# Performance work log

Measured on AMD Instinct MI355X. Metric: run time of the kernel, lower is better.

The kernel has to match this reference:

```python
import jax, jax.numpy as jnp
import numpy as np

B, LL, LP, D, H, TOPK = 4, 256, 256, 256, 128, 100


def setup_inputs() -> dict:
    key = jax.random.key(0)
    ks = jax.random.split(key, 16)
    s = 0.02
    return {
        "l_tok": jax.random.normal(ks[0], (B, LL, D), jnp.float32),
        "p_tok": jax.random.normal(ks[1], (B, LP, D), jnp.float32),
        "l_pad": jax.random.bernoulli(ks[2], 0.1, (B, LL)),
        "p_pad": jax.random.bernoulli(ks[3], 0.1, (B, LP)),
        "Wl": jax.random.normal(ks[4], (D, D), jnp.float32) * s,
        "bl": jnp.zeros((D,), jnp.float32),
        "Wp": jax.random.normal(ks[5], (D, D), jnp.float32) * s,
        "bp": jnp.zeros((D,), jnp.float32),
        "W1": jax.random.normal(ks[6], (H, 4 * D), jnp.float32) * s,
        "b1": jnp.zeros((H,), jnp.float32),
        "W2": jax.random.normal(ks[7], (H, H), jnp.float32) * s,
        "b2": jnp.zeros((H,), jnp.float32),
        "W3": jax.random.normal(ks[8], (1, H), jnp.float32) * s,
        "b3": jnp.zeros((1,), jnp.float32),
    }


def reference(l_tok, p_tok, l_pad, p_pad, Wl, bl, Wp, bp, W1, b1, W2, b2, W3, b3):
    # Linear projections (torch Linear: x @ W.T + b)
    l = jnp.einsum("bld,ed->ble", l_tok, Wl) + bl  # [B,Ll,D]
    p = jnp.einsum("bpd,ed->bpe", p_tok, Wp) + bp  # [B,Lp,D]

    le = jnp.broadcast_to(l[:, :, None, :], (B, LL, LP, D))
    pe = jnp.broadcast_to(p[:, None, :, :], (B, LL, LP, D))
    pair_feat = jnp.concatenate([le, pe, le * pe, jnp.abs(le - pe)], axis=-1)  # [B,Ll,Lp,4D]

    gelu = lambda x: jax.nn.gelu(x, approximate=False)  # torch nn.GELU default (erf)
    h = gelu(jnp.einsum("blpf,hf->blph", pair_feat, W1) + b1)
    h = gelu(jnp.einsum("blph,gh->blpg", h, W2) + b2)
    pair_logit = (jnp.einsum("blph,oh->blpo", h, W3) + b3)[..., 0]  # [B,Ll,Lp]

    pair_logit = jnp.nan_to_num(pair_logit, nan=0.0, posinf=20.0, neginf=-20.0)

    valid = (~l_pad)[:, :, None] & (~p_pad)[:, None, :]  # [B,Ll,Lp]
    pair_logit = jnp.where(valid, pair_logit, -20.0)
    pair_prob = jax.nn.sigmoid(pair_logit)

    flat = pair_logit.reshape(B, -1)
    k_top = min(TOPK, LL * LP)
    topv, _ = jax.lax.top_k(flat, k_top)  # [B,k]
    w = jax.nn.softmax(topv, axis=-1)
    logit = jnp.sum(w * topv, axis=-1)  # [B]
    return logit, pair_logit, pair_prob
```

## Files before the change

### kernel.cpp

```cpp
#include <hip/hip_runtime.h>

#define BB 4
#define LLL 256
#define LPP 256
#define DDIM 256
#define HH 128

typedef _Float16 f16;
typedef f16 f16x8 __attribute__((ext_vector_type(8)));
typedef f16 f16x4 __attribute__((ext_vector_type(4)));
typedef float floatx4 __attribute__((ext_vector_type(4)));

__device__ __forceinline__ float gelu_f(float x) {
    return x * __builtin_amdgcn_rcpf(1.f + __expf(-1.702f * x));
}
__device__ __forceinline__ float sigmoid_f(float x) {
    return __builtin_amdgcn_rcpf(1.f + __expf(-x));
}
__device__ __forceinline__ f16x8 habs8(f16x8 v) {
    uint4 u = __builtin_bit_cast(uint4, v);
    u.x &= 0x7fff7fffu; u.y &= 0x7fff7fffu; u.z &= 0x7fff7fffu; u.w &= 0x7fff7fffu;
    return __builtin_bit_cast(f16x8, u);
}
__device__ __forceinline__ unsigned okey(float f) {
    unsigned u = __float_as_uint(f);
    return (u & 0x80000000u) ? ~u : (u | 0x80000000u);
}

__global__ __launch_bounds__(256) void prep_proj(
    const float* __restrict__ l_tok, const float* __restrict__ p_tok,
    const float* __restrict__ Wl, const float* __restrict__ Wp,
    const float* __restrict__ bl, const float* __restrict__ bp,
    f16* __restrict__ proj) {
    __shared__ __align__(16) char sm[2 * 64 * 80];
    f16* As = (f16*)sm;
    f16* Bs = (f16*)(sm + 64 * 80);
    int tid = threadIdx.x;
    int m0 = blockIdx.x * 64, n0 = blockIdx.y * 64;
    bool isP = (m0 >= 1024);
    const float* Asrc = isP ? (p_tok + (size_t)(m0 - 1024) * DDIM) : (l_tok + (size_t)m0 * DDIM);
    const float* Wsrc = isP ? Wp : Wl;
    const float* bias = isP ? bp : bl;
    int row = tid >> 2, seg = tid & 3;
    int w = tid >> 6, lane = tid & 63;
    int m16 = lane & 15, quad = lane >> 4;
    int wm = w & 1, wn = w >> 1;
    floatx4 acc[2][2];
#pragma unroll
    for (int a = 0; a < 2; ++a)
#pragma unroll
        for (int c = 0; c < 2; ++c) acc[a][c] = (floatx4)0.f;
    for (int k0 = 0; k0 < DDIM; k0 += 32) {
        float4 f0 = *(const float4*)(Asrc + row * DDIM + k0 + seg * 8);
        float4 f1 = *(const float4*)(Asrc + row * DDIM + k0 + seg * 8 + 4);
        f16x8 av;
        av[0] = (f16)f0.x; av[1] = (f16)f0.y; av[2] = (f16)f0.z; av[3] = (f16)f0.w;
        av[4] = (f16)f1.x; av[5] = (f16)f1.y; av[6] = (f16)f1.z; av[7] = (f16)f1.w;
        *(f16x8*)(As + row * 40 + seg * 8) = av;
        float4 g0 = *(const float4*)(Wsrc + (n0 + row) * DDIM + k0 + seg * 8);
        float4 g1 = *(const float4*)(Wsrc + (n0 + row) * DDIM + k0 + seg * 8 + 4);
        f16x8 bv;
        bv[0] = (f16)g0.x; bv[1] = (f16)g0.y; bv[2] = (f16)g0.z; bv[3] = (f16)g0.w;
        bv[4] = (f16)g1.x; bv[5] = (f16)g1.y; bv[6] = (f16)g1.z; bv[7] = (f16)g1.w;
        *(f16x8*)(Bs + row * 40 + seg * 8) = bv;
        __syncthreads();
        f16x8 afr[2], bfr[2];
#pragma unroll
        for (int t = 0; t < 2; ++t)
            afr[t] = *(const f16x8*)(As + (wm * 32 + t * 16 + m16) * 40 + quad * 8);
#pragma unroll
        for (int t = 0; t < 2; ++t)
            bfr[t] = *(const f16x8*)(Bs + (wn * 32 + t * 16 + m16) * 40 + quad * 8);
#pragma unroll
        for (int a = 0; a < 2; ++a)
#pragma unroll
            for (int c = 0; c < 2; ++c)
                acc[a][c] = __builtin_amdgcn_mfma_f32_16x16x32_f16(afr[a], bfr[c], acc[a][c], 0, 0, 0);
        __syncthreads();
    }
#pragma unroll
    for (int c = 0; c < 2; ++c) {
        int col = n0 + wn * 32 + c * 16 + m16;
        float bv = bias[col];
#pragma unroll
        for (int a = 0; a < 2; ++a) {
            int rbase = m0 + wm * 32 + a * 16 + quad * 4;
#pragma unroll
            for (int i = 0; i < 4; ++i)
                proj[(size_t)(rbase + i) * DDIM + col] = (f16)(acc[a][c][i] + bv);
        }
    }
}

__global__ __launch_bounds__(256) void prep_ab(
    const f16* __restrict__ proj, const float* __restrict__ W1,
    const float* __restrict__ W2, float* __restrict__ ABt,
    f16* __restrict__ w1g, f16* __restrict__ w2g) {
    int tid = threadIdx.x;
    if (blockIdx.x >= 32) {
        int idx = ((blockIdx.x - 32) * 2 + blockIdx.y) * 256 + tid;
        if (idx < 8192) {
            int m16 = idx & 15, quad = (idx >> 4) & 3, th = (idx >> 6) & 7;
            int cd = (idx >> 9) & 1, ds = idx >> 10;
            int h = th * 16 + m16;
            const float* src = W1 + (size_t)h * 1024 + 512 + cd * 256 + ds * 32 + quad * 8;
            f16x8 v;
#pragma unroll
            for (int j = 0; j < 8; ++j) v[j] = (f16)src[j];
            *(f16x8*)(w1g + (size_t)idx * 8) = v;
        } else if (idx < 8192 + 2048) {
            int c = idx - 8192;
            int m16 = c & 15, quad = (c >> 4) & 3, tg = (c >> 6) & 7, ks = c >> 9;
            int g = tg * 16 + m16;
            f16x8 v;
#pragma unroll
            for (int j = 0; j < 8; ++j) v[j] = (f16)W2[g * HH + j * 16 + ks * 4 + quad];
            *(f16x8*)(w2g + (size_t)c * 8) = v;
        }
        return;
    }
    __shared__ __align__(16) char sm[2 * 64 * 80];
    f16* As = (f16*)sm;
    f16* Bs = (f16*)(sm + 64 * 80);
    int m0 = blockIdx.x * 64, n0 = blockIdx.y * 64;
    bool isP = (m0 >= 1024);
    int koff = isP ? 256 : 0;
    int row = tid >> 2, seg = tid & 3;
    int w = tid >> 6, lane = tid & 63;
    int m16 = lane & 15, quad = lane >> 4;
    int wm = w & 1, wn = w >> 1;
    floatx4 acc[2][2];
#pragma unroll
    for (int a = 0; a < 2; ++a)
#pragma unroll
        for (int c = 0; c < 2; ++c) acc[a][c] = (floatx4)0.f;
    for (int k0 = 0; k0 < DDIM; k0 += 32) {
        f16x8 av = *(const f16x8*)(proj + (size_t)(m0 + row) * DDIM + k0 + seg * 8);
        *(f16x8*)(As + row * 40 + seg * 8) = av;
        float4 g0 = *(const float4*)(W1 + (size_t)(n0 + row) * 1024 + koff + k0 + seg * 8);
        float4 g1 = *(const float4*)(W1 + (size_t)(n0 + row) * 1024 + koff + k0 + seg * 8 + 4);
        f16x8 bv;
        bv[0] = (f16)g0.x; bv[1] = (f16)g0.y; bv[2] = (f16)g0.z; bv[3] = (f16)g0.w;
        bv[4] = (f16)g1.x; bv[5] = (f16)g1.y; bv[6] = (f16)g1.z; bv[7] = (f16)g1.w;
        *(f16x8*)(Bs + row * 40 + seg * 8) = bv;
        __syncthreads();
        f16x8 afr[2], bfr[2];
#pragma unroll
        for (int t = 0; t < 2; ++t)
            afr[t] = *(const f16x8*)(As + (wm * 32 + t * 16 + m16) * 40 + quad * 8);
#pragma unroll
        for (int t = 0; t < 2; ++t)
            bfr[t] = *(const f16x8*)(Bs + (wn * 32 + t * 16 + m16) * 40 + quad * 8);
#pragma unroll
        for (int a = 0; a < 2; ++a)
#pragma unroll
            for (int c = 0; c < 2; ++c)
                acc[a][c] = __builtin_amdgcn_mfma_f32_16x16x32_f16(afr[a], bfr[c], acc[a][c], 0, 0, 0);
        __syncthreads();
    }
#pragma unroll
    for (int c = 0; c < 2; ++c) {
        int col = n0 + wn * 32 + c * 16 + m16;
#pragma unroll
        for (int a = 0; a < 2; ++a) {
            int rbase = m0 + wm * 32 + a * 16 + quad * 4;
#pragma unroll
            for (int i = 0; i < 4; ++i)
                ABt[(size_t)col * 2048 + rbase + i] = acc[a][c][i];
        }
    }
}

#define H1_STRIDE 272
#define SM_PLOG 139264
#define SM_TOTAL 141312

__global__ __launch_bounds__(512, 2) void pair_main(
    const f16* __restrict__ proj, const float* __restrict__ ABt,
    const f16* __restrict__ w1g, const f16* __restrict__ w2g,
    const float* __restrict__ b1, const float* __restrict__ b2,
    const float* __restrict__ W3, const float* __restrict__ b3,
    const int* __restrict__ l_pad, const int* __restrict__ p_pad,
    float* __restrict__ out) {
    __shared__ __align__(16) char sm[SM_TOTAL];
    int tid = threadIdx.x;
    int lane = tid & 63, w = tid >> 6;
    int m16 = lane & 15, quad = lane >> 4;
    int wp = w & 3, wh = w >> 2;
    int p0 = wp * 64, h0 = wh * 64;
    int b = blockIdx.y;
    int l0 = blockIdx.x * 2;
    int ml0 = b * LLL + l0;
    float* outPL = out + 4;
    float* outPR = out + 4 + BB * LLL * LPP;

    bool pad0 = (l_pad[ml0] != 0), pad1 = (l_pad[ml0 + 1] != 0);
    if (pad0 && pad1) {
        float pr = sigmoid_f(-20.f);
        if (tid < 512) {
            int j = tid >> 8, p = tid & 255;
            outPL[(size_t)(ml0 + j) * LPP + p] = -20.f;
            outPR[(size_t)(ml0 + j) * LPP + p] = pr;
        }
        return;
    }

    float* plog = (float*)(sm + SM_PLOG);

#pragma unroll
    for (int r = 0; r < 16; ++r) {
        int c = tid + r * 512;
        *(f16x8*)(sm + c * 16) = *(const f16x8*)(w1g + (size_t)c * 8);
    }
    if (tid < 512) plog[tid] = 0.f;

    floatx4 acc[2][4][4];
    {
        float av[2][4];
#pragma unroll
        for (int th = 0; th < 4; ++th) {
            int hh = h0 + th * 16 + m16;
            float base = b1[hh];
            av[0][th] = ABt[(size_t)hh * 2048 + ml0] + base;
            av[1][th] = ABt[(size_t)hh * 2048 + ml0 + 1] + base;
        }
#pragma unroll
        for (int tp = 0; tp < 4; ++tp) {
            int rp = p0 + tp * 16 + quad * 4;
#pragma unroll
            for (int th = 0; th < 4; ++th) {
                int hh = h0 + th * 16 + m16;
                floatx4 bp4 = *(const floatx4*)(ABt + (size_t)hh * 2048 + 1024 + b * LPP + rp);
#pragma unroll
                for (int j = 0; j < 2; ++j) {
                    floatx4 a;
#pragma unroll
                    for (int i = 0; i < 4; ++i) a[i] = bp4[i] + av[j][th];
                    acc[j][tp][th] = a;
                }
            }
        }
    }
    __syncthreads();

    {
        const f16* Lr0 = proj + (size_t)ml0 * DDIM + quad * 8;
        const f16* Lr1 = Lr0 + DDIM;
        const f16* Prl[4];
#pragma unroll
        for (int tp = 0; tp < 4; ++tp)
            Prl[tp] = proj + (size_t)(1024 + b * LPP + p0 + tp * 16 + m16) * DDIM + quad * 8;

        f16x8 lv0 = *(const f16x8*)(Lr0);
        f16x8 lv1 = *(const f16x8*)(Lr1);
        f16x8 pv[4];
#pragma unroll
        for (int tp = 0; tp < 4; ++tp) pv[tp] = *(const f16x8*)(Prl[tp]);

        for (int ds = 0; ds < 8; ++ds) {
            f16x8 nlv0, nlv1, npv[4];
            if (ds < 7) {
                nlv0 = *(const f16x8*)(Lr0 + (ds + 1) * 32);
                nlv1 = *(const f16x8*)(Lr1 + (ds + 1) * 32);
#pragma unroll
                for (int tp = 0; tp < 4; ++tp)
                    npv[tp] = *(const f16x8*)(Prl[tp] + (ds + 1) * 32);
            }
            const char* wb = sm + (size_t)(ds * 2) * 8192 + (wh * 4) * 1024 + quad * 256 + m16 * 16;
            {
                f16x8 x[2][4];
#pragma unroll
                for (int tp = 0; tp < 4; ++tp) {
                    x[0][tp] = lv0 * pv[tp];
                    x[1][tp] = lv1 * pv[tp];
                }
#pragma unroll
                for (int th = 0; th < 4; ++th) {
                    f16x8 bf = *(const f16x8*)(wb + th * 1024);
#pragma unroll
                    for (int j = 0; j < 2; ++j)
#pragma unroll
                        for (int tp = 0; tp < 4; ++tp)
                            acc[j][tp][th] = __builtin_amdgcn_mfma_f32_16x16x32_f16(x[j][tp], bf, acc[j][tp][th], 0, 0, 0);
                }
            }
            {
                f16x8 x[2][4];
#pragma unroll
                for (int tp = 0; tp < 4; ++tp) {
                    x[0][tp] = habs8(lv0 - pv[tp]);
                    x[1][tp] = habs8(lv1 - pv[tp]);
                }
#pragma unroll
                for (int th = 0; th < 4; ++th) {
                    f16x8 bf = *(const f16x8*)(wb + 8192 + th * 1024);
#pragma unroll
                    for (int j = 0; j < 2; ++j)
#pragma unroll
                        for (int tp = 0; tp < 4; ++tp)
                            acc[j][tp][th] = __builtin_amdgcn_mfma_f32_16x16x32_f16(x[j][tp], bf, acc[j][tp][th], 0, 0, 0);
                }
            }
            lv0 = nlv0; lv1 = nlv1;
#pragma unroll
            for (int tp = 0; tp < 4; ++tp) pv[tp] = npv[tp];
        }
    }
    __syncthreads();

#pragma unroll
    for (int j = 0; j < 2; ++j) {
        char* h1s = sm + j * (256 * H1_STRIDE);
#pragma unroll
        for (int tp = 0; tp < 4; ++tp) {
#pragma unroll
            for (int i = 0; i < 4; ++i) {
                f16x4 hv;
#pragma unroll
                for (int th = 0; th < 4; ++th) hv[th] = (f16)gelu_f(acc[j][tp][th][i]);
                int p = p0 + tp * 16 + quad * 4 + i;
                *(f16x4*)(h1s + p * H1_STRIDE + m16 * 16 + wh * 8) = hv;
            }
        }
    }
    __syncthreads();

    float b2v[4], w3v[4];
#pragma unroll
    for (int th = 0; th < 4; ++th) {
        int g = h0 + th * 16 + m16;
        b2v[th] = b2[g];
        w3v[th] = W3[g];
    }
    floatx4 acc2[2][4][4];
#pragma unroll
    for (int j = 0; j < 2; ++j)
#pragma unroll
        for (int tp = 0; tp < 4; ++tp)
#pragma unroll
            for (int th = 0; th < 4; ++th) {
                floatx4 a;
                a[0] = a[1] = a[2] = a[3] = b2v[th];
                acc2[j][tp][th] = a;
            }
#pragma unroll
    for (int ks = 0; ks < 4; ++ks) {
        f16x8 af[2][4];
#pragma unroll
        for (int j = 0; j < 2; ++j)
#pragma unroll
            for (int tp = 0; tp < 4; ++tp)
                af[j][tp] = *(const f16x8*)(sm + j * (256 * H1_STRIDE) +
                                            (p0 + tp * 16 + m16) * H1_STRIDE + ks * 64 + quad * 16);
#pragma unroll
        for (int th = 0; th < 4; ++th) {
            f16x8 bf = *(const f16x8*)(w2g + (size_t)(((ks * 8 + wh * 4 + th) * 4 + quad) * 16 + m16) * 8);
#pragma unroll
            for (int j = 0; j < 2; ++j)
#pragma unroll
                for (int tp = 0; tp < 4; ++tp)
                    acc2[j][tp][th] = __builtin_amdgcn_mfma_f32_16x16x32_f16(af[j][tp], bf, acc2[j][tp][th], 0, 0, 0);
        }
    }

#pragma unroll
    for (int j = 0; j < 2; ++j) {
        float part[16];
#pragma unroll
        for (int q = 0; q < 16; ++q) part[q] = 0.f;
#pragma unroll
        for (int tp = 0; tp < 4; ++tp)
#pragma unroll
            for (int th = 0; th < 4; ++th)
#pragma unroll
                for (int i = 0; i < 4; ++i)
                    part[tp * 4 + i] += w3v[th] * gelu_f(acc2[j][tp][th][i]);
#pragma unroll
        for (int mask = 1; mask <= 8; mask <<= 1)
#pragma unroll
            for (int q = 0; q < 16; ++q) part[q] += __shfl_xor(part[q], mask, 64);
        if (m16 == 0) {
#pragma unroll
            for (int tp = 0; tp < 4; ++tp)
#pragma unroll
                for (int i = 0; i < 4; ++i)
                    atomicAdd(&plog[j * 256 + p0 + tp * 16 + quad * 4 + i], part[tp * 4 + i]);
        }
    }
    __syncthreads();

    if (tid < 512) {
        int j = tid >> 8, p = tid & 255;
        int ml = ml0 + j;
        float pl;
        if (l_pad[ml] != 0) {
            pl = -20.f;
        } else {
            pl = plog[tid] + b3[0];
            if (__builtin_isnan(pl)) pl = 0.f;
            else if (__builtin_isinf(pl)) pl = pl > 0.f ? 20.f : -20.f;
            if (p_pad[b * LPP + p] != 0) pl = -20.f;
        }
        outPL[(size_t)ml * LPP + p] = pl;
        outPR[(size_t)ml * LPP + p] = sigmoid_f(pl);
    }
}

#define TK_H0(b) (tk + (b) * 256)
#define TK_H1(b) (tk + 1024 + (b) * 256)
#define TK_SEL(b) (tk + 2048 + (b) * 4)
#define TK_S1(b) ((float*)(tk + 2064) + (b))
#define TK_S2(b) ((float*)(tk + 2068 + 12) + (b))
#define TK_INTS 2096

__global__ __launch_bounds__(256) void tk_hist0(const float* __restrict__ pl,
                                                int* __restrict__ tk) {
    __shared__ int h[256];
    int tid = threadIdx.x, b = blockIdx.y;
    h[tid] = 0;
    __syncthreads();
    float4 t = ((const float4*)(pl + (size_t)b * 65536 + blockIdx.x * 1024))[tid];
#pragma unroll
    for (int c = 0; c < 4; ++c) atomicAdd(&h[okey((&t.x)[c]) >> 24], 1);
    __syncthreads();
    if (h[tid]) atomicAdd(&TK_H0(b)[tid], h[tid]);
}

__global__ __launch_bounds__(256) void tk_sel(int* __restrict__ tk, int level) {
    __shared__ int s[257];
    int tid = threadIdx.x, b = blockIdx.x;
    const int* hsrc = level ? TK_H1(b) : TK_H0(b);
    int K = level ? TK_SEL(b)[1] : 100;
    s[tid] = hsrc[tid];
    __syncthreads();
    for (int off = 1; off < 256; off <<= 1) {
        int v = (tid + off < 256) ? s[tid + off] : 0;
        __syncthreads();
        s[tid] += v;
        __syncthreads();
    }
    int nxt = (tid < 255) ? s[tid + 1] : 0;
    if (s[tid] >= K && nxt < K) {
        TK_SEL(b)[level * 2] = tid;
        TK_SEL(b)[level * 2 + 1] = K - nxt;
    }
}

__global__ __launch_bounds__(256) void tk_pass1(const float* __restrict__ pl,
                                                int* __restrict__ tk) {
    __shared__ int h[256];
    __shared__ float red[8];
    int tid = threadIdx.x, b = blockIdx.y;
    int lane = tid & 63, wv = tid >> 6;
    unsigned pref0 = (unsigned)TK_SEL(b)[0];
    h[tid] = 0;
    __syncthreads();
    float4 t = ((const float4*)(pl + (size_t)b * 65536 + blockIdx.x * 1024))[tid];
    float s1 = 0.f, s2 = 0.f;
#pragma unroll
    for (int c = 0; c < 4; ++c) {
        float v = (&t.x)[c];
        unsigned key = okey(v);
        unsigned hi = key >> 24;
        if (hi > pref0) {
            float e = __expf(v);
            s1 += e;
            s2 += e * v;
        } else if (hi == pref0) {
            atomicAdd(&h[(key >> 16) & 255], 1);
        }
    }
    __syncthreads();
    if (h[tid]) atomicAdd(&TK_H1(b)[tid], h[tid]);
    for (int off = 32; off > 0; off >>= 1) {
        s1 += __shfl_xor(s1, off, 64);
        s2 += __shfl_xor(s2, off, 64);
    }
    if (lane == 0) { red[wv] = s1; red[4 + wv] = s2; }
    __syncthreads();
    if (tid == 0) {
        float a = red[0] + red[1] + red[2] + red[3];
        float bsum = red[4] + red[5] + red[6] + red[7];
        if (a != 0.f) {
            atomicAdd(TK_S1(b), a);
            atomicAdd(TK_S2(b), bsum);
        }
    }
}

__global__ __launch_bounds__(256) void tk_pass2(const float* __restrict__ pl,
                                                int* __restrict__ tk) {
    __shared__ float red[8];
    int tid = threadIdx.x, b = blockIdx.y;
    int lane = tid & 63, wv = tid >> 6;
    unsigned pref0 = (unsigned)TK_SEL(b)[0];
    unsigned pref1 = (unsigned)TK_SEL(b)[2];
    float4 t = ((const float4*)(pl + (size_t)b * 65536 + blockIdx.x * 1024))[tid];
    float s1 = 0.f, s2 = 0.f;
#pragma unroll
    for (int c = 0; c < 4; ++c) {
        float v = (&t.x)[c];
        unsigned key = okey(v);
        if ((key >> 24) == pref0 && ((key >> 16) & 255) > pref1) {
            float e = __expf(v);
            s1 += e;
            s2 += e * v;
        }
    }
    for (int off = 32; off > 0; off >>= 1) {
        s1 += __shfl_xor(s1, off, 64);
        s2 += __shfl_xor(s2, off, 64);
    }
    if (lane == 0) { red[wv] = s1; red[4 + wv] = s2; }
    __syncthreads();
    if (tid == 0) {
        float a = red[0] + red[1] + red[2] + red[3];
        float bsum = red[4] + red[5] + red[6] + red[7];
        if (a != 0.f) {
            atomicAdd(TK_S1(b), a);
            atomicAdd(TK_S2(b), bsum);
        }
    }
}

__global__ __launch_bounds__(64) void tk_fin(int* __restrict__ tk,
                                             float* __restrict__ out) {
    int b = threadIdx.x;
    if (b >= BB) return;
    unsigned pref0 = (unsigned)TK_SEL(b)[0];
    unsigned pref1 = (unsigned)TK_SEL(b)[2];
    int rem1 = TK_SEL(b)[3];
    unsigned key = (pref0 << 24) | (pref1 << 16) | 0x8000u;
    unsigned bits = (key & 0x80000000u) ? (key & 0x7fffffffu) : ~key;
    float vT = __uint_as_float(bits);
    float e = __expf(vT);
    float s1 = *TK_S1(b) + (float)rem1 * e;
    float s2 = *TK_S2(b) + (float)rem1 * e * vT;
    out[b] = s2 * __builtin_amdgcn_rcpf(s1);
}

extern "C" void kernel_launch(void* const* d_in, const int* in_sizes, int n_in,
                              void* d_out, int out_size, void* d_ws, size_t ws_size,
                              hipStream_t stream) {
    const float* l_tok = (const float*)d_in[0];
    const float* p_tok = (const float*)d_in[1];
    const int* l_pad = (const int*)d_in[2];
    const int* p_pad = (const int*)d_in[3];
    const float* Wl = (const float*)d_in[4];
    const float* bl = (const float*)d_in[5];
    const float* Wp = (const float*)d_in[6];
    const float* bp = (const float*)d_in[7];
    const float* W1 = (const float*)d_in[8];
    const float* b1 = (const float*)d_in[9];
    const float* W2 = (const float*)d_in[10];
    const float* b2 = (const float*)d_in[11];
    const float* W3 = (const float*)d_in[12];
    const float* b3 = (const float*)d_in[13];
    float* out = (float*)d_out;

    char* ws = (char*)d_ws;
    f16* proj = (f16*)ws;
    float* ABt = (float*)(ws + (size_t)2048 * 256 * 2);
    f16* w1g = (f16*)(ws + (size_t)2048 * 256 * 2 + (size_t)128 * 2048 * 4);
    f16* w2g = (f16*)((char*)w1g + (size_t)8192 * 16);
    int* tk = (int*)((char*)w2g + (size_t)2048 * 16);

    hipMemsetAsync(tk, 0, TK_INTS * sizeof(int), stream);
    prep_proj<<<dim3(32, 4), 256, 0, stream>>>(l_tok, p_tok, Wl, Wp, bl, bp, proj);
    prep_ab<<<dim3(52, 2), 256, 0, stream>>>(proj, W1, W2, ABt, w1g, w2g);
    pair_main<<<dim3(LLL / 2, BB), 512, 0, stream>>>(proj, ABt, w1g, w2g, b1, b2, W3, b3,
                                                     l_pad, p_pad, out);
    const float* pl = out + 4;
    tk_hist0<<<dim3(64, BB), 256, 0, stream>>>(pl, tk);
    tk_sel<<<BB, 256, 0, stream>>>(tk, 0);
    tk_pass1<<<dim3(64, BB), 256, 0, stream>>>(pl, tk);
    tk_sel<<<BB, 256, 0, stream>>>(tk, 1);
    tk_pass2<<<dim3(64, BB), 256, 0, stream>>>(pl, tk);
    tk_fin<<<1, 64, 0, stream>>>(tk, out);
}
```

Baseline: 178.1 us.

## Fuse top-k histogram into pair kernel and collapse select/finalize launches

The first-level radix histogram moves into pair_main, which builds a per-block shared-memory histogram and flushes it with global atomics. The prefix-scan select step is recomputed redundantly inside each tk_pass block, so the separate tk_hist0, tk_sel and tk_fin kernels are dropped. The final softmax-weighted sum is done by the last block of tk_pass2 using a completion counter, and the workspace memset is folded into extra prep_ab blocks. This removes several small launches and one full re-read of pair_logit, at the cost of extra shared-memory atomics and LDS in the main kernel plus repeated scans in every top-k block.

```diff
diff --git a/kernel.cpp b/kernel.cpp
--- a/kernel.cpp
+++ b/kernel.cpp
@@ -26,6 +26,13 @@
     unsigned u = __float_as_uint(f);
     return (u & 0x80000000u) ? ~u : (u | 0x80000000u);
 }
+
+#define TK_H0(b) (tk + (b) * 256)
+#define TK_H1(b) (tk + 1024 + (b) * 256)
+#define TK_S1(b) ((float*)(tk + 2048) + (b))
+#define TK_S2(b) ((float*)(tk + 2052) + (b))
+#define TK_CNT(b) (tk + 2056 + (b))
+#define TK_INTS 2060
 
 __global__ __launch_bounds__(256) void prep_proj(
     const float* __restrict__ l_tok, const float* __restrict__ p_tok,
@@ -95,7 +102,7 @@
 __global__ __launch_bounds__(256) void prep_ab(
     const f16* __restrict__ proj, const float* __restrict__ W1,
     const float* __restrict__ W2, float* __restrict__ ABt,
-    f16* __restrict__ w1g, f16* __restrict__ w2g) {
+    f16* __restrict__ w1g, f16* __restrict__ w2g, int* __restrict__ tk) {
     int tid = threadIdx.x;
     if (blockIdx.x >= 32) {
         int idx = ((blockIdx.x - 32) * 2 + blockIdx.y) * 256 + tid;
@@ -116,6 +123,9 @@
 #pragma unroll
             for (int j = 0; j < 8; ++j) v[j] = (f16)W2[g * HH + j * 16 + ks * 4 + quad];
             *(f16x8*)(w2g + (size_t)c * 8) = v;
+        } else {
+            int zid = idx - 10240;
+            if (zid >= 0 && zid < TK_INTS) tk[zid] = 0;
         }
         return;
     }
@@ -173,7 +183,8 @@
 
 #define H1_STRIDE 272
 #define SM_PLOG 139264
-#define SM_TOTAL 141312
+#define SM_HIST 141312
+#define SM_TOTAL 142336
 
 __global__ __launch_bounds__(512, 2) void pair_main(
     const f16* __restrict__ proj, const float* __restrict__ ABt,
@@ -181,7 +192,7 @@
     const float* __restrict__ b1, const float* __restrict__ b2,
     const float* __restrict__ W3, const float* __restrict__ b3,
     const int* __restrict__ l_pad, const int* __restrict__ p_pad,
-    float* __restrict__ out) {
+    float* __restrict__ out, int* __restrict__ tk) {
     __shared__ __align__(16) char sm[SM_TOTAL];
     int tid = threadIdx.x;
     int lane = tid & 63, w = tid >> 6;
@@ -202,10 +213,12 @@
             outPL[(size_t)(ml0 + j) * LPP + p] = -20.f;
             outPR[(size_t)(ml0 + j) * LPP + p] = pr;
         }
+        if (tid == 0) atomicAdd(&TK_H0(b)[okey(-20.f) >> 24], 512);
         return;
     }
 
     float* plog = (float*)(sm + SM_PLOG);
+    int* lhist = (int*)(sm + SM_HIST);
 
 #pragma unroll
     for (int r = 0; r < 16; ++r) {
@@ -213,6 +226,7 @@
         *(f16x8*)(sm + c * 16) = *(const f16x8*)(w1g + (size_t)c * 8);
     }
     if (tid < 512) plog[tid] = 0.f;
+    if (tid < 256) lhist[tid] = 0;
 
     floatx4 acc[2][4][4];
     {
@@ -403,58 +417,33 @@
         }
         outPL[(size_t)ml * LPP + p] = pl;
         outPR[(size_t)ml * LPP + p] = sigmoid_f(pl);
-    }
-}
-
-#define TK_H0(b) (tk + (b) * 256)
-#define TK_H1(b) (tk + 1024 + (b) * 256)
-#define TK_SEL(b) (tk + 2048 + (b) * 4)
-#define TK_S1(b) ((float*)(tk + 2064) + (b))
-#define TK_S2(b) ((float*)(tk + 2068 + 12) + (b))
-#define TK_INTS 2096
-
-__global__ __launch_bounds__(256) void tk_hist0(const float* __restrict__ pl,
-                                                int* __restrict__ tk) {
-    __shared__ int h[256];
-    int tid = threadIdx.x, b = blockIdx.y;
-    h[tid] = 0;
-    __syncthreads();
-    float4 t = ((const float4*)(pl + (size_t)b * 65536 + blockIdx.x * 1024))[tid];
-#pragma unroll
-    for (int c = 0; c < 4; ++c) atomicAdd(&h[okey((&t.x)[c]) >> 24], 1);
-    __syncthreads();
-    if (h[tid]) atomicAdd(&TK_H0(b)[tid], h[tid]);
-}
-
-__global__ __launch_bounds__(256) void tk_sel(int* __restrict__ tk, int level) {
-    __shared__ int s[257];
-    int tid = threadIdx.x, b = blockIdx.x;
-    const int* hsrc = level ? TK_H1(b) : TK_H0(b);
-    int K = level ? TK_SEL(b)[1] : 100;
-    s[tid] = hsrc[tid];
-    __syncthreads();
-    for (int off = 1; off < 256; off <<= 1) {
-        int v = (tid + off < 256) ? s[tid + off] : 0;
-        __syncthreads();
-        s[tid] += v;
-        __syncthreads();
-    }
-    int nxt = (tid < 255) ? s[tid + 1] : 0;
-    if (s[tid] >= K && nxt < K) {
-        TK_SEL(b)[level * 2] = tid;
-        TK_SEL(b)[level * 2 + 1] = K - nxt;
-    }
+        atomicAdd(&lhist[okey(pl) >> 24], 1);
+    }
+    __syncthreads();
+    if (tid < 256 && lhist[tid]) atomicAdd(&TK_H0(b)[tid], lhist[tid]);
 }
 
 __global__ __launch_bounds__(256) void tk_pass1(const float* __restrict__ pl,
                                                 int* __restrict__ tk) {
+    __shared__ int s[257];
     __shared__ int h[256];
     __shared__ float red[8];
     int tid = threadIdx.x, b = blockIdx.y;
     int lane = tid & 63, wv = tid >> 6;
-    unsigned pref0 = (unsigned)TK_SEL(b)[0];
+    s[tid] = TK_H0(b)[tid];
     h[tid] = 0;
     __syncthreads();
+    for (int off = 1; off < 256; off <<= 1) {
+        int v = (tid + off < 256) ? s[tid + off] : 0;
+        __syncthreads();
+        s[tid] += v;
+        __syncthreads();
+    }
+    int nxt = (tid < 255) ? s[tid + 1] : 0;
+    if (s[tid] >= 100 && nxt < 100) s[256] = tid;
+    __syncthreads();
+    unsigned pref0 = (unsigned)s[256];
+
     float4 t = ((const float4*)(pl + (size_t)b * 65536 + blockIdx.x * 1024))[tid];
     float s1 = 0.f, s2 = 0.f;
 #pragma unroll
@@ -489,12 +478,44 @@
 }
 
 __global__ __launch_bounds__(256) void tk_pass2(const float* __restrict__ pl,
-                                                int* __restrict__ tk) {
+                                                int* __restrict__ tk,
+                                                float* __restrict__ out) {
+    __shared__ int s[258];
     __shared__ float red[8];
     int tid = threadIdx.x, b = blockIdx.y;
     int lane = tid & 63, wv = tid >> 6;
-    unsigned pref0 = (unsigned)TK_SEL(b)[0];
-    unsigned pref1 = (unsigned)TK_SEL(b)[2];
+    s[tid] = TK_H0(b)[tid];
+    __syncthreads();
+    for (int off = 1; off < 256; off <<= 1) {
+        int v = (tid + off < 256) ? s[tid + off] : 0;
+        __syncthreads();
+        s[tid] += v;
+        __syncthreads();
+    }
+    {
+        int nxt = (tid < 255) ? s[tid + 1] : 0;
+        if (s[tid] >= 100 && nxt < 100) { s[256] = tid; s[257] = 100 - nxt; }
+    }
+    __syncthreads();
+    unsigned pref0 = (unsigned)s[256];
+    int rem0 = s[257];
+    __syncthreads();
+    s[tid] = TK_H1(b)[tid];
+    __syncthreads();
+    for (int off = 1; off < 256; off <<= 1) {
+        int v = (tid + off < 256) ? s[tid + off] : 0;
+        __syncthreads();
+        s[tid] += v;
+        __syncthreads();
+    }
+    {
+        int nxt = (tid < 255) ? s[tid + 1] : 0;
+        if (s[tid] >= rem0 && nxt < rem0) { s[256] = tid; s[257] = rem0 - nxt; }
+    }
+    __syncthreads();
+    unsigned pref1 = (unsigned)s[256];
+    int rem1 = s[257];
+
     float4 t = ((const float4*)(pl + (size_t)b * 65536 + blockIdx.x * 1024))[tid];
     float s1 = 0.f, s2 = 0.f;
 #pragma unroll
@@ -520,23 +541,20 @@
             atomicAdd(TK_S1(b), a);
             atomicAdd(TK_S2(b), bsum);
         }
-    }
-}
-
-__global__ __launch_bounds__(64) void tk_fin(int* __restrict__ tk,
-                                             float* __restrict__ out) {
-    int b = threadIdx.x;
-    if (b >= BB) return;
-    unsigned pref0 = (unsigned)TK_SEL(b)[0];
-    unsigned pref1 = (unsigned)TK_SEL(b)[2];
-    int rem1 = TK_SEL(b)[3];
-    unsigned key = (pref0 << 24) | (pref1 << 16) | 0x8000u;
-    unsigned bits = (key & 0x80000000u) ? (key & 0x7fffffffu) : ~key;
-    float vT = __uint_as_float(bits);
-    float e = __expf(vT);
-    float s1 = *TK_S1(b) + (float)rem1 * e;
-    float s2 = *TK_S2(b) + (float)rem1 * e * vT;
-    out[b] = s2 * __builtin_amdgcn_rcpf(s1);
+        __threadfence();
+        int done = atomicAdd(TK_CNT(b), 1);
+        if (done == gridDim.x - 1) {
+            float S1 = atomicAdd(TK_S1(b), 0.f);
+            float S2 = atomicAdd(TK_S2(b), 0.f);
+            unsigned key = (pref0 << 24) | (pref1 << 16) | 0x8000u;
+            unsigned bits = (key & 0x80000000u) ? (key & 0x7fffffffu) : ~key;
+            float vT = __uint_as_float(bits);
+            float e = __expf(vT);
+            S1 += (float)rem1 * e;
+            S2 += (float)rem1 * e * vT;
+            out[b] = S2 * __builtin_amdgcn_rcpf(S1);
+        }
+    }
 }
 
 extern "C" void kernel_launch(void* const* d_in, const int* in_sizes, int n_in,
@@ -565,16 +583,11 @@
     f16* w2g = (f16*)((char*)w1g + (size_t)8192 * 16);
     int* tk = (int*)((char*)w2g + (size_t)2048 * 16);
 
-    hipMemsetAsync(tk, 0, TK_INTS * sizeof(int), stream);
     prep_proj<<<dim3(32, 4), 256, 0, stream>>>(l_tok, p_tok, Wl, Wp, bl, bp, proj);
-    prep_ab<<<dim3(52, 2), 256, 0, stream>>>(proj, W1, W2, ABt, w1g, w2g);
+    prep_ab<<<dim3(57, 2), 256, 0, stream>>>(proj, W1, W2, ABt, w1g, w2g, tk);
     pair_main<<<dim3(LLL / 2, BB), 512, 0, stream>>>(proj, ABt, w1g, w2g, b1, b2, W3, b3,
-                                                     l_pad, p_pad, out);
+                                                     l_pad, p_pad, out, tk);
     const float* pl = out + 4;
-    tk_hist0<<<dim3(64, BB), 256, 0, stream>>>(pl, tk);
-    tk_sel<<<BB, 256, 0, stream>>>(tk, 0);
     tk_pass1<<<dim3(64, BB), 256, 0, stream>>>(pl, tk);
-    tk_sel<<<BB, 256, 0, stream>>>(tk, 1);
-    tk_pass2<<<dim3(64, BB), 256, 0, stream>>>(pl, tk);
-    tk_fin<<<1, 64, 0, stream>>>(tk, out);
-}
+    tk_pass2<<<dim3(64, BB), 256, 0, stream>>>(pl, tk, out);
+}
```

Measured after the change: 178.9 us. Within noise of the previous version (+0.5%).
